# Kernel tuning notes

Hardware: AMD Instinct MI355X
Metric: run time of the kernel (lower is better)

The kernel has to match this reference:

```python
import jax, jax.numpy as jnp
import numpy as np

B, N, M, K = 2, 50000, 50000, 16
C_IN, C_ADD, C_MID = 64, 3, 16


def setup_inputs() -> dict:
    key = jax.random.key(0)
    k1, k2, k3, k4 = jax.random.split(key, 4)
    return {
        "input_features": jax.random.normal(k1, (B, N, C_IN), dtype=jnp.float32),
        "neighbor_inds": jax.random.randint(k2, (B, M, K), 0, N, dtype=jnp.int64),
        "weightnet": jax.random.normal(k3, (B, M, K, C_MID), dtype=jnp.float32),
        "additional_features": jax.random.normal(k4, (B, M, K, C_ADD), dtype=jnp.float32),
    }


def reference(input_features, neighbor_inds, weightnet, additional_features):
    # Gather neighbor features: [B, M, K, C_in]
    gathered = jax.vmap(lambda feat, idx: feat[idx])(input_features, neighbor_inds)
    # Concatenate additional per-neighbor features: [B, M, K, C_in + C_add]
    cat = jnp.concatenate([gathered, additional_features], axis=-1)
    # Weighted reduce over neighbors: [B, M, C_total, C_mid]
    out = jnp.einsum("bmkc,bmkw->bmcw", cat, weightnet)
    b, m = out.shape[:2]
    return out.reshape(b, m, -1)
```

## Files before the change

kernel.cpp:

```cpp
#include <hip/hip_runtime.h>
#include <cstdint>
#include <cstddef>


namespace {
constexpr int B_   = 2;
constexpr int N_   = 50000;
constexpr int M_   = 50000;
constexpr int KNB  = 16;
constexpr int CIN  = 64;
constexpr int COUT = 67 * 16;
constexpr int PAIRS = B_ * M_;
constexpr int FELEMS = B_ * N_ * CIN;
}

typedef unsigned int u32;
typedef float  f32x4   __attribute__((ext_vector_type(4)));
typedef short  short8  __attribute__((ext_vector_type(8)));
typedef short  short4v __attribute__((ext_vector_type(4)));
typedef u32    u32x4   __attribute__((ext_vector_type(4)));
typedef u32    u32x2   __attribute__((ext_vector_type(2)));

struct IdxS   { int v[16]; };
struct StageG { u32 bg[4][4]; float wf[4]; float ad[4]; };
struct StageF { float bg[4][8]; float ad[8]; float wf[8]; };

static __device__ __forceinline__ short8 pack_bf8(const float* x) {
  u32x4 w;
  #pragma unroll
  for (int q = 0; q < 4; ++q)
    w[q] = __builtin_amdgcn_perm(__builtin_bit_cast(u32, x[2*q+1]),
                                 __builtin_bit_cast(u32, x[2*q]),
                                 0x07060302u);
  return __builtin_bit_cast(short8, w);
}

static __device__ __forceinline__ short4v pack_bf4(const float* x) {
  u32x2 w;
  #pragma unroll
  for (int q = 0; q < 2; ++q)
    w[q] = __builtin_amdgcn_perm(__builtin_bit_cast(u32, x[2*q+1]),
                                 __builtin_bit_cast(u32, x[2*q]),
                                 0x07060302u);
  return __builtin_bit_cast(short4v, w);
}

static __device__ __forceinline__ u32 bfrne(float x) {
  u32 u = __builtin_bit_cast(u32, x);
  return (u + 0x7FFFu + ((u >> 16) & 1u)) >> 16;
}

__global__ __launch_bounds__(256)
void cvt_feat_bf16(const float* __restrict__ src, unsigned short* __restrict__ dst) {
  const int n4 = FELEMS / 4;
  int i = blockIdx.x * blockDim.x + threadIdx.x;
  const int stride = gridDim.x * blockDim.x;
  const f32x4* s4 = reinterpret_cast<const f32x4*>(src);
  for (; i < n4; i += stride) {
    f32x4 v = s4[i];
    u32x2 w;
    w[0] = bfrne(v[0]) | (bfrne(v[1]) << 16);
    w[1] = bfrne(v[2]) | (bfrne(v[3]) << 16);
    *reinterpret_cast<u32x2*>(dst + 4 * (size_t)i) = w;
  }
}

static __device__ __forceinline__ void load_idx(const int* __restrict__ idxp, IdxS& r) {
  #pragma unroll
  for (int j = 0; j < 16; ++j)
    r.v[j] = __builtin_amdgcn_readfirstlane(idxp[j]);
}

#if __has_builtin(__builtin_amdgcn_mfma_f32_16x16x16bf16_1k)

static __device__ __forceinline__ void issue_loads(const unsigned short* __restrict__ tbl,
                                                   const float* __restrict__ wnet,
                                                   const float* __restrict__ addf,
                                                   int q, const IdxS& I,
                                                   int cc, int g1, int g2, int g,
                                                   StageG& S) {
  const unsigned short* __restrict__ fb =
      tbl + ((q >= M_) ? (size_t)N_ * CIN : 0);
  const float* __restrict__ wnp = wnet + (size_t)q * 256;
  const float* __restrict__ adp = addf + (size_t)q * 48;

  int row[4];
  #pragma unroll
  for (int j = 0; j < 4; ++j) {
    const int ra = g1 ? I.v[4 + j]  : I.v[j];
    const int rb = g1 ? I.v[12 + j] : I.v[8 + j];
    row[j] = g2 ? rb : ra;
  }
  #pragma unroll
  for (int j = 0; j < 4; ++j) {
    const unsigned short* __restrict__ rp = fb + (((u32)row[j]) << 6) + (u32)cc;
    #pragma unroll
    for (int t = 0; t < 4; ++t)
      S.bg[t][j] = rp[t * 16];
  }
  const float* __restrict__ wp = wnp + g * 64 + cc;
  #pragma unroll
  for (int j = 0; j < 4; ++j)
    S.wf[j] = __builtin_nontemporal_load(wp + j * 16);
  const float* __restrict__ ap = adp + g * 12 + cc;
  #pragma unroll
  for (int j = 0; j < 4; ++j)
    S.ad[j] = (cc < 3) ? __builtin_nontemporal_load(ap + j * 3) : 0.f;
}

static __device__ __forceinline__ void compute_store(const StageG& S,
                                                     float* __restrict__ op,
                                                     int cc, int g) {
  const int soff = cc * 16 + g * 4;
  const short4v a = pack_bf4(S.wf);
  #pragma unroll
  for (int t = 0; t < 4; ++t) {
    u32x2 w;
    w[0] = S.bg[t][0] | (S.bg[t][1] << 16);
    w[1] = S.bg[t][2] | (S.bg[t][3] << 16);
    const short4v bb = __builtin_bit_cast(short4v, w);
    f32x4 acc = {0.f, 0.f, 0.f, 0.f};
    acc = __builtin_amdgcn_mfma_f32_16x16x16bf16_1k(a, bb, acc, 0, 0, 0);
    __builtin_nontemporal_store(acc, reinterpret_cast<f32x4*>(op + soff + t * 256));
  }
  {
    const short4v bb = pack_bf4(S.ad);
    f32x4 acc = {0.f, 0.f, 0.f, 0.f};
    acc = __builtin_amdgcn_mfma_f32_16x16x16bf16_1k(a, bb, acc, 0, 0, 0);
    if (cc < 3)
      __builtin_nontemporal_store(acc, reinterpret_cast<f32x4*>(op + soff + 1024));
  }
}

__global__ __launch_bounds__(256, 4)
void pconv11(const unsigned short* __restrict__ tbl, const int* __restrict__ inds,
             const float* __restrict__ wnet, const float* __restrict__ addf,
             float* __restrict__ out)
{
  const int lane = threadIdx.x & 63;
  const int cc = lane & 15, g = lane >> 4;
  const int g1 = g & 1, g2 = g >> 1;
  const int gw = __builtin_amdgcn_readfirstlane(
      (int)((blockIdx.x * blockDim.x + threadIdx.x) >> 6));
  const int nw = (int)((gridDim.x * blockDim.x) >> 6);
  if (gw >= PAIRS) return;

  IdxS iA, iB, iC;
  StageG sA, sB, sC;
  int p = gw;

  load_idx(inds + (size_t)p * KNB, iA);
  { const int q = (p + nw < PAIRS) ? (p + nw) : gw;
    load_idx(inds + (size_t)q * KNB, iB); }
  { const int q = (p + 2 * nw < PAIRS) ? (p + 2 * nw) : gw;
    load_idx(inds + (size_t)q * KNB, iC); }
  issue_loads(tbl, wnet, addf, p, iA, cc, g1, g2, g, sA);
  { const int q = (p + nw < PAIRS) ? (p + nw) : gw;
    issue_loads(tbl, wnet, addf, q, iB, cc, g1, g2, g, sB); }

  while (true) {
    {
      const int q2 = (p + 2 * nw < PAIRS) ? (p + 2 * nw) : gw;
      issue_loads(tbl, wnet, addf, q2, iC, cc, g1, g2, g, sC);
      const int q3 = (p + 3 * nw < PAIRS) ? (p + 3 * nw) : gw;
      load_idx(inds + (size_t)q3 * KNB, iA);
      compute_store(sA, out + (size_t)p * COUT, cc, g);
      p += nw; if (p >= PAIRS) break;
    }
    {
      const int q2 = (p + 2 * nw < PAIRS) ? (p + 2 * nw) : gw;
      issue_loads(tbl, wnet, addf, q2, iA, cc, g1, g2, g, sA);
      const int q3 = (p + 3 * nw < PAIRS) ? (p + 3 * nw) : gw;
      load_idx(inds + (size_t)q3 * KNB, iB);
      compute_store(sB, out + (size_t)p * COUT, cc, g);
      p += nw; if (p >= PAIRS) break;
    }
    {
      const int q2 = (p + 2 * nw < PAIRS) ? (p + 2 * nw) : gw;
      issue_loads(tbl, wnet, addf, q2, iB, cc, g1, g2, g, sB);
      const int q3 = (p + 3 * nw < PAIRS) ? (p + 3 * nw) : gw;
      load_idx(inds + (size_t)q3 * KNB, iC);
      compute_store(sC, out + (size_t)p * COUT, cc, g);
      p += nw; if (p >= PAIRS) break;
    }
  }
}

#else

struct StageT { unsigned short bg[4][8]; float ad[8]; float wf[8]; };

static __device__ __forceinline__ void load_stage_t(const unsigned short* __restrict__ fb,
                                                    const float* __restrict__ wnp,
                                                    const float* __restrict__ adp,
                                                    const IdxS& I, int lane, StageT& S) {
  const int cc = lane & 15;
  if (lane < 32) {
    const int hi = lane >> 4;
    int rows[8];
    #pragma unroll
    for (int j = 0; j < 8; ++j) rows[j] = hi ? I.v[j + 8] : I.v[j];
    #pragma unroll
    for (int j = 0; j < 8; ++j) {
      const u32 rb = ((u32)rows[j]) << 6;
      #pragma unroll
      for (int t = 0; t < 4; ++t)
        S.bg[t][j] = fb[rb + (u32)(t * 16 + cc)];
    }
    const u32 woff = (hi ? 128u : 0u) + (u32)cc;
    #pragma unroll
    for (int j = 0; j < 8; ++j)
      S.wf[j] = __builtin_nontemporal_load(wnp + woff + j * 16);
    if (cc < 3) {
      const u32 aoff = (hi ? 24u : 0u) + (u32)cc;
      #pragma unroll
      for (int j = 0; j < 8; ++j)
        S.ad[j] = __builtin_nontemporal_load(adp + aoff + j * 3);
    }
  }
}

__global__ __launch_bounds__(256, 4)
void pconv11(const unsigned short* __restrict__ tbl, const int* __restrict__ inds,
             const float* __restrict__ wnet, const float* __restrict__ addf,
             float* __restrict__ out)
{
  const int lane = threadIdx.x & 63;
  const int gw = __builtin_amdgcn_readfirstlane(
      (int)((blockIdx.x * blockDim.x + threadIdx.x) >> 6));
  const int nw = (int)((gridDim.x * blockDim.x) >> 6);
  if (gw >= PAIRS) return;

  IdxS iCur, iNext;
  load_idx(inds + (size_t)gw * KNB, iCur);
  for (int p = gw; p < PAIRS; p += nw) {
    const int pn = (p + nw < PAIRS) ? (p + nw) : gw;
    load_idx(inds + (size_t)pn * KNB, iNext);
    const int b = (p >= M_) ? 1 : 0;
    StageT S = {};
    load_stage_t(tbl + (size_t)b * N_ * CIN, wnet + (size_t)p * 256,
                 addf + (size_t)p * 48, iCur, lane, S);
    const int cc = lane & 15, g = lane >> 4;
    const int soff = cc * 16 + g * 4;
    float* op = out + (size_t)p * COUT;
    const short8 a = pack_bf8(S.wf);
    #pragma unroll
    for (int t = 0; t < 4; ++t) {
      short8 bb;
      #pragma unroll
      for (int j = 0; j < 8; ++j) bb[j] = (short)S.bg[t][j];
      f32x4 acc = {0.f, 0.f, 0.f, 0.f};
      acc = __builtin_amdgcn_mfma_f32_16x16x32_bf16(a, bb, acc, 0, 0, 0);
      __builtin_nontemporal_store(acc, reinterpret_cast<f32x4*>(op + soff + t * 256));
    }
    {
      const short8 bb = pack_bf8(S.ad);
      f32x4 acc = {0.f, 0.f, 0.f, 0.f};
      acc = __builtin_amdgcn_mfma_f32_16x16x32_bf16(a, bb, acc, 0, 0, 0);
      if (cc < 3)
        __builtin_nontemporal_store(acc, reinterpret_cast<f32x4*>(op + soff + 1024));
    }
    #pragma unroll
    for (int j = 0; j < 16; ++j) iCur.v[j] = iNext.v[j];
  }
}

#endif

static __device__ __forceinline__ void load_stage_f(const float* __restrict__ fb,
                                                    const float* __restrict__ wnp,
                                                    const float* __restrict__ adp,
                                                    const IdxS& I, int lane, StageF& S) {
  const int cc = lane & 15;
  if (lane < 32) {
    const int hi = lane >> 4;
    int rows[8];
    #pragma unroll
    for (int j = 0; j < 8; ++j) rows[j] = hi ? I.v[j + 8] : I.v[j];
    #pragma unroll
    for (int j = 0; j < 8; ++j) {
      const u32 rb = ((u32)rows[j]) << 6;
      #pragma unroll
      for (int t = 0; t < 4; ++t)
        S.bg[t][j] = fb[rb + (u32)(t * 16 + cc)];
    }
    const u32 woff = (hi ? 128u : 0u) + (u32)cc;
    #pragma unroll
    for (int j = 0; j < 8; ++j)
      S.wf[j] = __builtin_nontemporal_load(wnp + woff + j * 16);
    if (cc < 3) {
      const u32 aoff = (hi ? 24u : 0u) + (u32)cc;
      #pragma unroll
      for (int j = 0; j < 8; ++j)
        S.ad[j] = __builtin_nontemporal_load(adp + aoff + j * 3);
    }
  }
}

__global__ __launch_bounds__(256, 4)
void pconv11_f32(const float* __restrict__ feat, const int* __restrict__ inds,
                 const float* __restrict__ wnet, const float* __restrict__ addf,
                 float* __restrict__ out)
{
  const int lane = threadIdx.x & 63;
  const int gw = __builtin_amdgcn_readfirstlane(
      (int)((blockIdx.x * blockDim.x + threadIdx.x) >> 6));
  const int nw = (int)((gridDim.x * blockDim.x) >> 6);
  if (gw >= PAIRS) return;

  IdxS iCur, iNext;
  load_idx(inds + (size_t)gw * KNB, iCur);
  for (int p = gw; p < PAIRS; p += nw) {
    const int pn = (p + nw < PAIRS) ? (p + nw) : gw;
    load_idx(inds + (size_t)pn * KNB, iNext);
    const int b = (p >= M_) ? 1 : 0;
    StageF S = {};
    load_stage_f(feat + (size_t)b * N_ * CIN, wnet + (size_t)p * 256,
                 addf + (size_t)p * 48, iCur, lane, S);
    const int cc = lane & 15, g = lane >> 4;
    const int soff = cc * 16 + g * 4;
    float* op = out + (size_t)p * COUT;
    const short8 a = pack_bf8(S.wf);
    #pragma unroll
    for (int t = 0; t < 4; ++t) {
      const short8 bb = pack_bf8(S.bg[t]);
      f32x4 acc = {0.f, 0.f, 0.f, 0.f};
      acc = __builtin_amdgcn_mfma_f32_16x16x32_bf16(a, bb, acc, 0, 0, 0);
      __builtin_nontemporal_store(acc, reinterpret_cast<f32x4*>(op + soff + t * 256));
    }
    {
      const short8 bb = pack_bf8(S.ad);
      f32x4 acc = {0.f, 0.f, 0.f, 0.f};
      acc = __builtin_amdgcn_mfma_f32_16x16x32_bf16(a, bb, acc, 0, 0, 0);
      if (cc < 3)
        __builtin_nontemporal_store(acc, reinterpret_cast<f32x4*>(op + soff + 1024));
    }
    #pragma unroll
    for (int j = 0; j < 16; ++j) iCur.v[j] = iNext.v[j];
  }
}

extern "C" void kernel_launch(void* const* d_in, const int* in_sizes, int n_in,
                              void* d_out, int out_size, void* d_ws, size_t ws_size,
                              hipStream_t stream) {
  const float* feat = (const float*)d_in[0];
  const int*   inds = (const int*)d_in[1];
  const float* wnet = (const float*)d_in[2];
  const float* addf = (const float*)d_in[3];
  float* outp = (float*)d_out;

  const size_t TBL_BYTES = (size_t)FELEMS * sizeof(unsigned short);

  dim3 grid(4096), block(256);
  if (ws_size >= TBL_BYTES) {
    unsigned short* tbl = (unsigned short*)d_ws;
    hipLaunchKernelGGL(cvt_feat_bf16, dim3(2048), dim3(256), 0, stream, feat, tbl);
    hipLaunchKernelGGL(pconv11, grid, block, 0, stream, tbl, inds, wnet, addf, outp);
  } else {
    hipLaunchKernelGGL(pconv11_f32, grid, block, 0, stream,
                       feat, inds, wnet, addf, outp);
  }
}
```

Baseline: 158.6 us.

## Deepen gather software pipeline to four stages and shrink grid to 1024 blocks

```diff
diff --git a/kernel.cpp b/kernel.cpp
--- a/kernel.cpp
+++ b/kernel.cpp
@@ -132,8 +132,10 @@
   }
 }
 
+#define CLAMP_P(x) (((x) < PAIRS) ? (x) : gw)
+
 __global__ __launch_bounds__(256, 4)
-void pconv11(const unsigned short* __restrict__ tbl, const int* __restrict__ inds,
+void pconv12(const unsigned short* __restrict__ tbl, const int* __restrict__ inds,
              const float* __restrict__ wnet, const float* __restrict__ addf,
              float* __restrict__ out)
 {
@@ -145,46 +147,47 @@
   const int nw = (int)((gridDim.x * blockDim.x) >> 6);
   if (gw >= PAIRS) return;
 
-  IdxS iA, iB, iC;
-  StageG sA, sB, sC;
+  IdxS iA, iB, iC, iD;
+  StageG sA, sB, sC, sD;
   int p = gw;
 
-  load_idx(inds + (size_t)p * KNB, iA);
-  { const int q = (p + nw < PAIRS) ? (p + nw) : gw;
-    load_idx(inds + (size_t)q * KNB, iB); }
-  { const int q = (p + 2 * nw < PAIRS) ? (p + 2 * nw) : gw;
-    load_idx(inds + (size_t)q * KNB, iC); }
-  issue_loads(tbl, wnet, addf, p, iA, cc, g1, g2, g, sA);
-  { const int q = (p + nw < PAIRS) ? (p + nw) : gw;
-    issue_loads(tbl, wnet, addf, q, iB, cc, g1, g2, g, sB); }
+  load_idx(inds + (size_t)CLAMP_P(p) * KNB, iA);
+  load_idx(inds + (size_t)CLAMP_P(p + nw) * KNB, iB);
+  load_idx(inds + (size_t)CLAMP_P(p + 2 * nw) * KNB, iC);
+  load_idx(inds + (size_t)CLAMP_P(p + 3 * nw) * KNB, iD);
+  issue_loads(tbl, wnet, addf, CLAMP_P(p),          iA, cc, g1, g2, g, sA);
+  issue_loads(tbl, wnet, addf, CLAMP_P(p + nw),     iB, cc, g1, g2, g, sB);
+  issue_loads(tbl, wnet, addf, CLAMP_P(p + 2 * nw), iC, cc, g1, g2, g, sC);
 
   while (true) {
     {
-      const int q2 = (p + 2 * nw < PAIRS) ? (p + 2 * nw) : gw;
-      issue_loads(tbl, wnet, addf, q2, iC, cc, g1, g2, g, sC);
-      const int q3 = (p + 3 * nw < PAIRS) ? (p + 3 * nw) : gw;
-      load_idx(inds + (size_t)q3 * KNB, iA);
+      issue_loads(tbl, wnet, addf, CLAMP_P(p + 3 * nw), iD, cc, g1, g2, g, sD);
+      load_idx(inds + (size_t)CLAMP_P(p + 4 * nw) * KNB, iA);
       compute_store(sA, out + (size_t)p * COUT, cc, g);
       p += nw; if (p >= PAIRS) break;
     }
     {
-      const int q2 = (p + 2 * nw < PAIRS) ? (p + 2 * nw) : gw;
-      issue_loads(tbl, wnet, addf, q2, iA, cc, g1, g2, g, sA);
-      const int q3 = (p + 3 * nw < PAIRS) ? (p + 3 * nw) : gw;
-      load_idx(inds + (size_t)q3 * KNB, iB);
+      issue_loads(tbl, wnet, addf, CLAMP_P(p + 3 * nw), iA, cc, g1, g2, g, sA);
+      load_idx(inds + (size_t)CLAMP_P(p + 4 * nw) * KNB, iB);
       compute_store(sB, out + (size_t)p * COUT, cc, g);
       p += nw; if (p >= PAIRS) break;
     }
     {
-      const int q2 = (p + 2 * nw < PAIRS) ? (p + 2 * nw) : gw;
-      issue_loads(tbl, wnet, addf, q2, iB, cc, g1, g2, g, sB);
-      const int q3 = (p + 3 * nw < PAIRS) ? (p + 3 * nw) : gw;
-      load_idx(inds + (size_t)q3 * KNB, iC);
+      issue_loads(tbl, wnet, addf, CLAMP_P(p + 3 * nw), iB, cc, g1, g2, g, sB);
+      load_idx(inds + (size_t)CLAMP_P(p + 4 * nw) * KNB, iC);
       compute_store(sC, out + (size_t)p * COUT, cc, g);
       p += nw; if (p >= PAIRS) break;
     }
-  }
-}
+    {
+      issue_loads(tbl, wnet, addf, CLAMP_P(p + 3 * nw), iC, cc, g1, g2, g, sC);
+      load_idx(inds + (size_t)CLAMP_P(p + 4 * nw) * KNB, iD);
+      compute_store(sD, out + (size_t)p * COUT, cc, g);
+      p += nw; if (p >= PAIRS) break;
+    }
+  }
+}
+
+#undef CLAMP_P
 
 #else
 
@@ -221,7 +224,7 @@
 }
 
 __global__ __launch_bounds__(256, 4)
-void pconv11(const unsigned short* __restrict__ tbl, const int* __restrict__ inds,
+void pconv12(const unsigned short* __restrict__ tbl, const int* __restrict__ inds,
              const float* __restrict__ wnet, const float* __restrict__ addf,
              float* __restrict__ out)
 {
@@ -298,7 +301,7 @@
 }
 
 __global__ __launch_bounds__(256, 4)
-void pconv11_f32(const float* __restrict__ feat, const int* __restrict__ inds,
+void pconv12_f32(const float* __restrict__ feat, const int* __restrict__ inds,
                  const float* __restrict__ wnet, const float* __restrict__ addf,
                  float* __restrict__ out)
 {
@@ -351,13 +354,13 @@
 
   const size_t TBL_BYTES = (size_t)FELEMS * sizeof(unsigned short);
 
-  dim3 grid(4096), block(256);
+  dim3 grid(1024), block(256);
   if (ws_size >= TBL_BYTES) {
     unsigned short* tbl = (unsigned short*)d_ws;
     hipLaunchKernelGGL(cvt_feat_bf16, dim3(2048), dim3(256), 0, stream, feat, tbl);
-    hipLaunchKernelGGL(pconv11, grid, block, 0, stream, tbl, inds, wnet, addf, outp);
+    hipLaunchKernelGGL(pconv12, grid, block, 0, stream, tbl, inds, wnet, addf, outp);
   } else {
-    hipLaunchKernelGGL(pconv11_f32, grid, block, 0, stream,
+    hipLaunchKernelGGL(pconv12_f32, grid, block, 0, stream,
                        feat, inds, wnet, addf, outp);
   }
 }
```

Result: faster. 153.3 us (-3.4%).
